# Kernel optimization log

Measured on AMD Instinct MI355X. Metric: run time of the kernel, lower is better.

The kernel has to match this reference:

```python
import jax, jax.numpy as jnp
import numpy as np

DIM = 768
H = 12          # num_heads
HD = DIM // H   # head_dim = 64
WS = 128        # window_size
SHIFT = 64      # shift_size
NPATCH = 128    # num_patches for relative bias
MLP = 3072
EPS = 1e-5


def _layernorm(x, w, b):
    m = jnp.mean(x, axis=-1, keepdims=True)
    v = jnp.mean(jnp.square(x - m), axis=-1, keepdims=True)
    return (x - m) * jax.lax.rsqrt(v + EPS) * w + b


def _window_attention(xw, mw, qkv_w, qkv_b, proj_w, proj_b, rel_bias):
    # xw: [Bw, ws, C] windows, mw: [Bw, ws] bool valid-key mask
    Bw, N, C = xw.shape
    qkv = (xw @ qkv_w + qkv_b).reshape(Bw, N, 3, H, HD)
    qkv = jnp.transpose(qkv, (2, 0, 3, 1, 4))  # [3, Bw, H, N, hd]
    q, k, v = qkv[0], qkv[1], qkv[2]
    attn = jnp.einsum('bhqd,bhkd->bhqk', q, k) * (HD ** -0.5)
    # relative position bias: table [2*NPATCH-1, H] gathered by index [N, N]
    coords = jnp.arange(N)
    rel_idx = coords[None, :] - coords[:, None] + (NPATCH - 1)  # [N, N]
    bias = jnp.transpose(rel_bias[rel_idx], (2, 0, 1))  # [H, N, N]
    attn = attn + bias[None]
    neg = jnp.finfo(attn.dtype).min
    attn = jnp.where(mw[:, None, None, :], attn, neg)  # mask invalid keys
    attn = jax.nn.softmax(attn, axis=-1)
    attn = jnp.nan_to_num(attn, nan=0.0)
    out = jnp.einsum('bhqk,bhkd->bqhd', attn, v).reshape(Bw, N, C)
    return out @ proj_w + proj_b


def reference(x, norm1_w, norm1_b, qkv_w, qkv_b, proj_w, proj_b, rel_bias,
              ls1, norm2_w, norm2_b, fc1_w, fc1_b, fc2_w, fc2_b, ls2):
    B, N, C = x.shape
    # ---- attention branch: norm1 -> shifted-window attention ----
    h = _layernorm(x, norm1_w, norm1_b)
    pad = (-N) % WS
    hp = jnp.pad(h, ((0, 0), (0, pad), (0, 0)))  # zero-pad sequence
    Npad = N + pad
    valid = jnp.broadcast_to(jnp.arange(Npad) < N, (B, Npad))
    if SHIFT > 0:
        hp = jnp.roll(hp, -SHIFT, axis=1)
        valid = jnp.roll(valid, -SHIFT, axis=1)
    nw = Npad // WS
    xw = hp.reshape(B * nw, WS, C)
    mw = valid.reshape(B * nw, WS)
    aw = _window_attention(xw, mw, qkv_w, qkv_b, proj_w, proj_b, rel_bias)
    a = aw.reshape(B, Npad, C)
    if SHIFT > 0:
        a = jnp.roll(a, SHIFT, axis=1)
    a = a[:, :N, :]
    x = x + a * ls1  # LayerScale, DropPath is identity
    # ---- MLP branch ----
    h2 = _layernorm(x, norm2_w, norm2_b)
    m = jax.nn.gelu(h2 @ fc1_w + fc1_b, approximate=False) @ fc2_w + fc2_b
    return x + m * ls2


def setup_inputs() -> dict:
    key = jax.random.key(0)
    ks = jax.random.split(key, 8)
    B, N = 16, 2000
    s = 0.02
    return {
        'x': jax.random.normal(ks[0], (B, N, DIM), jnp.float32),
        'norm1_w': jnp.ones((DIM,), jnp.float32),
        'norm1_b': jnp.zeros((DIM,), jnp.float32),
        'qkv_w': s * jax.random.normal(ks[1], (DIM, 3 * DIM), jnp.float32),
        'qkv_b': jnp.zeros((3 * DIM,), jnp.float32),
        'proj_w': s * jax.random.normal(ks[2], (DIM, DIM), jnp.float32),
        'proj_b': jnp.zeros((DIM,), jnp.float32),
        'rel_bias': s * jax.random.normal(ks[3], (2 * NPATCH - 1, H), jnp.float32),
        'ls1': 1e-5 * jnp.ones((DIM,), jnp.float32),
        'norm2_w': jnp.ones((DIM,), jnp.float32),
        'norm2_b': jnp.zeros((DIM,), jnp.float32),
        'fc1_w': s * jax.random.normal(ks[4], (DIM, MLP), jnp.float32),
        'fc1_b': jnp.zeros((MLP,), jnp.float32),
        'fc2_w': s * jax.random.normal(ks[5], (MLP, DIM), jnp.float32),
        'fc2_b': jnp.zeros((DIM,), jnp.float32),
        'ls2': 1e-5 * jnp.ones((DIM,), jnp.float32),
    }
```

## Files before the change

### kernel.cpp

```cpp
#include <hip/hip_runtime.h>
#include <hip/hip_bf16.h>

typedef unsigned short u16;
typedef unsigned char u8;
typedef __attribute__((ext_vector_type(8))) short bh8;
typedef __attribute__((ext_vector_type(4))) float fx4;
typedef __attribute__((ext_vector_type(4))) int i32x4;
typedef __attribute__((ext_vector_type(8))) int i32x8;

__device__ __forceinline__ u16 f2bf(float f) {
  union { float f; unsigned u; } v; v.f = f;
  unsigned r = v.u + 0x7FFFu + ((v.u >> 16) & 1u);
  return (u16)(r >> 16);
}

__device__ __forceinline__ u8 f2fp8(float x) {
  union { float f; unsigned u; } v; v.f = x;
  const unsigned sign = (v.u >> 24) & 0x80u;
  v.u &= 0x7FFFFFFFu;
  if (v.f >= 464.0f) return (u8)(sign | 0x7Eu);
  if (v.f < 0.015625f) {
    int q = (int)rintf(v.f * 512.0f);
    return (u8)(sign | (unsigned)q);
  }
  unsigned u2 = v.u + 0x7FFFFu + ((v.u >> 20) & 1u);
  unsigned e2 = (u2 >> 23) - 127u + 7u;
  unsigned mant = (u2 >> 20) & 7u;
  return (u8)(sign | (e2 << 3) | mant);
}

__device__ __forceinline__ void cvt2_fp8(float a, float b, u8& x, u8& y) {
#if __has_builtin(__builtin_amdgcn_cvt_pk_fp8_f32)
  int r = __builtin_amdgcn_cvt_pk_fp8_f32(a, b, 0, false);
  x = (u8)(r & 0xff);
  y = (u8)((r >> 8) & 0xff);
#else
  x = f2fp8(a);
  y = f2fp8(b);
#endif
}

__device__ __forceinline__ void gload_lds16(const void* g, void* l) {
  __builtin_amdgcn_global_load_lds(
      (const __attribute__((address_space(1))) void*)g,
      (__attribute__((address_space(3))) void*)l, 16, 0, 0);
}

__device__ __forceinline__ i32x8 rd32(const char* p0, const char* p1) {
  i32x4 lo = *(const i32x4*)p0;
  i32x4 hi = *(const i32x4*)p1;
  return __builtin_shufflevector(lo, hi, 0, 1, 2, 3, 4, 5, 6, 7);
}

__global__ __launch_bounds__(256) void transp_cvt(
    const float* __restrict__ W, u8* __restrict__ Wt, int K, int N) {
  __shared__ float tile[32][33];
  const int k0 = blockIdx.x * 32, n0 = blockIdx.y * 32;
  const int tx = threadIdx.x & 31, ty = threadIdx.x >> 5;
#pragma unroll
  for (int i = 0; i < 4; ++i)
    tile[ty + i * 8][tx] = W[(size_t)(k0 + ty + i * 8) * N + n0 + tx];
  __syncthreads();
#pragma unroll
  for (int i = 0; i < 4; ++i)
    Wt[(size_t)(n0 + ty + i * 8) * K + k0 + tx] = f2fp8(tile[tx][ty + i * 8] * 32.0f);
}

__device__ __forceinline__ float blockSum(float v, float* sh) {
#pragma unroll
  for (int m = 32; m; m >>= 1) v += __shfl_xor(v, m);
  if ((threadIdx.x & 63) == 0) sh[threadIdx.x >> 6] = v;
  __syncthreads();
  return sh[0] + sh[1] + sh[2] + sh[3];
}

__global__ __launch_bounds__(256) void ln1_k(
    const float* __restrict__ x, const float* __restrict__ w,
    const float* __restrict__ b, u8* __restrict__ hw) {
  __shared__ float sh1[4], sh2[4];
  const int row = blockIdx.x;
  const int bI = row >> 11, i = row & 2047;
  const int j = (i + 64) & 2047;
  const int tid = threadIdx.x;
  u8* dst = hw + (size_t)row * 768;
  if (j >= 2000) {
    dst[tid] = 0; dst[tid + 256] = 0; dst[tid + 512] = 0;
    return;
  }
  const float* xr = x + ((size_t)bI * 2000 + j) * 768;
  float v0 = xr[tid], v1 = xr[tid + 256], v2 = xr[tid + 512];
  float mean = blockSum(v0 + v1 + v2, sh1) * (1.0f / 768.0f);
  float d0 = v0 - mean, d1 = v1 - mean, d2 = v2 - mean;
  float var = blockSum(d0 * d0 + d1 * d1 + d2 * d2, sh2) * (1.0f / 768.0f);
  float rs = rsqrtf(var + 1e-5f);
  u8 x0, x1, x2, xd;
  cvt2_fp8((d0 * rs * w[tid] + b[tid]) * 4.0f,
           (d1 * rs * w[tid + 256] + b[tid + 256]) * 4.0f, x0, x1);
  cvt2_fp8((d2 * rs * w[tid + 512] + b[tid + 512]) * 4.0f, 0.0f, x2, xd);
  dst[tid] = x0; dst[tid + 256] = x1; dst[tid + 512] = x2;
}

__global__ __launch_bounds__(256) void ln2_k(
    const float* __restrict__ src, const float* __restrict__ w,
    const float* __restrict__ b, u8* __restrict__ dsth) {
  __shared__ float sh1[4], sh2[4];
  const int row = blockIdx.x;
  const int tid = threadIdx.x;
  const float* xr = src + (size_t)row * 768;
  u8* dst = dsth + (size_t)row * 768;
  float v0 = xr[tid], v1 = xr[tid + 256], v2 = xr[tid + 512];
  float mean = blockSum(v0 + v1 + v2, sh1) * (1.0f / 768.0f);
  float d0 = v0 - mean, d1 = v1 - mean, d2 = v2 - mean;
  float var = blockSum(d0 * d0 + d1 * d1 + d2 * d2, sh2) * (1.0f / 768.0f);
  float rs = rsqrtf(var + 1e-5f);
  u8 x0, x1, x2, xd;
  cvt2_fp8((d0 * rs * w[tid] + b[tid]) * 4.0f,
           (d1 * rs * w[tid + 256] + b[tid + 256]) * 4.0f, x0, x1);
  cvt2_fp8((d2 * rs * w[tid + 512] + b[tid + 512]) * 4.0f, 0.0f, x2, xd);
  dst[tid] = x0; dst[tid + 256] = x1; dst[tid + 512] = x2;
}

enum { EQKV = 0, EPROJ = 1, EFC1 = 2, EFC2 = 3 };

template <int EPI>
__global__ __launch_bounds__(256, 3) void gemm128f8(
    const u8* __restrict__ A, const u8* __restrict__ Bt,
    const float* __restrict__ bias, const float* __restrict__ lsv,
    const float* __restrict__ resid, float* __restrict__ outf,
    u16* __restrict__ outh, u8* __restrict__ outb,
    int gn, int N, int K, int mValid) {
  __shared__ u8 LDSBUF[32768];
  u8* As = LDSBUF;
  u8* Bs = LDSBUF + 16384;
  const int tid = threadIdx.x;
  const int lane = tid & 63, wid = tid >> 6;
  const int wr = wid >> 1, wc = wid & 1;

  const int nwg = gridDim.x, bid = blockIdx.x;
  const int q = nwg >> 3, r = nwg & 7;
  const int xcd = bid & 7, idx = bid >> 3;
  const int wg = (xcd < r ? xcd * (q + 1) : r * (q + 1) + (xcd - r) * q) + idx;
  const int mt = wg / gn, nt = wg % gn;
  const int m0 = mt * 128, n0 = nt * 128;
  const int NT = K >> 7;

  fx4 acc[4][4];
#pragma unroll
  for (int i = 0; i < 4; ++i)
#pragma unroll
    for (int j = 0; j < 4; ++j) acc[i][j] = fx4{0.f, 0.f, 0.f, 0.f};

  const int rsel = lane & 15, kgrp = lane >> 4;
  const int colb = kgrp * 32;
  const int xorc = (rsel & 7) << 4;

  const int rl = tid >> 3;
  const int kc16 = ((tid & 7) ^ (rl & 7)) * 16;
  const u8* aRow = A + (size_t)(m0 + rl) * K + kc16;
  const u8* bRow = Bt + (size_t)(n0 + rl) * K + kc16;

  for (int t = 0; t < NT; ++t) {
    const int k0 = t << 7;
#pragma unroll
    for (int i = 0; i < 4; ++i) {
      gload_lds16(aRow + (size_t)k0 + (size_t)(i * 32) * K,
                  (char*)As + i * 4096 + wid * 1024);
      gload_lds16(bRow + (size_t)k0 + (size_t)(i * 32) * K,
                  (char*)Bs + i * 4096 + wid * 1024);
    }
    __syncthreads();
    i32x8 af[4];
#pragma unroll
    for (int mi = 0; mi < 4; ++mi) {
      const char* ab = (const char*)As + (wr * 64 + mi * 16 + rsel) * 128;
      af[mi] = rd32(ab + (colb ^ xorc), ab + ((colb + 16) ^ xorc));
    }
#pragma unroll
    for (int ni = 0; ni < 4; ++ni) {
      const char* bb = (const char*)Bs + (wc * 64 + ni * 16 + rsel) * 128;
      i32x8 bfr = rd32(bb + (colb ^ xorc), bb + ((colb + 16) ^ xorc));
#pragma unroll
      for (int mi = 0; mi < 4; ++mi)
        acc[mi][ni] = __builtin_amdgcn_mfma_scale_f32_16x16x128_f8f6f4(
            af[mi], bfr, acc[mi][ni], 0, 0, 0, 125, 0, 122);
    }
    __syncthreads();
  }

  const int cc = lane & 15;
  const int rq = (lane >> 4) * 4;

  if (EPI == EQKV) {
    u16* Ls = (u16*)LDSBUF;
#pragma unroll
    for (int ni = 0; ni < 4; ++ni) {
      const int col = wc * 64 + ni * 16 + cc;
      const float bv = bias[n0 + col];
#pragma unroll
      for (int mi = 0; mi < 4; ++mi)
#pragma unroll
        for (int j = 0; j < 4; ++j)
          Ls[(wr * 64 + mi * 16 + rq + j) * 128 + col] = f2bf(acc[mi][ni][j] + bv);
    }
    __syncthreads();
#pragma unroll
    for (int i = 0; i < 8; ++i) {
      const int row = i * 16 + (tid >> 4);
      i32x4 v = *(const i32x4*)(LDSBUF + row * 256 + (tid & 15) * 16);
      *(i32x4*)(outh + (size_t)(m0 + row) * N + n0 + (tid & 15) * 8) = v;
    }
  } else if (EPI == EFC1) {
    u8* Ls = LDSBUF;
#pragma unroll
    for (int ni = 0; ni < 4; ++ni) {
      const int col = wc * 64 + ni * 16 + cc;
      const float bv = bias[n0 + col];
#pragma unroll
      for (int mi = 0; mi < 4; ++mi) {
#pragma unroll
        for (int jp = 0; jp < 2; ++jp) {
          const float va = acc[mi][ni][jp * 2] + bv;
          const float vb = acc[mi][ni][jp * 2 + 1] + bv;
          const float ga = va / (1.0f + __expf(-1.702f * va)) * 4.0f;
          const float gb = vb / (1.0f + __expf(-1.702f * vb)) * 4.0f;
          u8 xa, xb;
          cvt2_fp8(ga, gb, xa, xb);
          const int row = wr * 64 + mi * 16 + rq + jp * 2;
          Ls[row * 128 + col] = xa;
          Ls[(row + 1) * 128 + col] = xb;
        }
      }
    }
    __syncthreads();
#pragma unroll
    for (int i = 0; i < 4; ++i) {
      const int row = i * 32 + (tid >> 3);
      i32x4 v = *(const i32x4*)(Ls + row * 128 + (tid & 7) * 16);
      *(i32x4*)(outb + (size_t)(m0 + row) * N + n0 + (tid & 7) * 16) = v;
    }
  } else {
    float* Lf = (float*)LDSBUF;
#pragma unroll
    for (int p = 0; p < 2; ++p) {
      if (p) __syncthreads();
      if (wc == p) {
#pragma unroll
        for (int ni = 0; ni < 4; ++ni) {
          const int gc = n0 + p * 64 + ni * 16 + cc;
          const float bv = bias[gc], ls = lsv[gc];
#pragma unroll
          for (int mi = 0; mi < 4; ++mi)
#pragma unroll
            for (int j = 0; j < 4; ++j)
              Lf[(wr * 64 + mi * 16 + rq + j) * 64 + ni * 16 + cc] =
                  (acc[mi][ni][j] + bv) * ls;
        }
      }
      __syncthreads();
#pragma unroll
      for (int i = 0; i < 8; ++i) {
        const int row = i * 16 + (tid >> 4);
        const int gr = m0 + row;
        fx4 s = *(const fx4*)(Lf + row * 64 + (tid & 15) * 4);
        if (EPI == EFC2) {
          if (gr < mValid) {
            float* po = outf + (size_t)gr * 768 + n0 + p * 64 + (tid & 15) * 4;
            fx4 cur = *(const fx4*)po;
            *(fx4*)po = fx4{cur[0] + s[0], cur[1] + s[1], cur[2] + s[2], cur[3] + s[3]};
          }
        } else {
          const int bI = gr >> 11, ip = gr & 2047;
          const int jj = (ip + 64) & 2047;
          if (jj < 2000) {
            const size_t o = ((size_t)bI * 2000 + jj) * 768 + n0 + p * 64 + (tid & 15) * 4;
            fx4 rv = *(const fx4*)(resid + o);
            *(fx4*)(outf + o) = fx4{rv[0] + s[0], rv[1] + s[1], rv[2] + s[2], rv[3] + s[3]};
          }
        }
      }
    }
  }
}

struct AttnLds {
  union {
    struct { u16 Qs[128][72]; u16 Ks[128][72]; } qk;
    u16 Ps[128][136];
  } u;
  u16 Vt[64][136];
  float biasv[256];
};

__global__ __launch_bounds__(256, 2) void attn_k(
    const u16* __restrict__ qkv, const float* __restrict__ rel_bias,
    u8* __restrict__ aout) {
  __shared__ AttnLds L;
  const int blk = blockIdx.x;
  const int w = blk / 12, h = blk - w * 12;
  const int wi = w & 15;
  const int tid = threadIdx.x;
  const int lane = tid & 63, wid = tid >> 6;

  if (tid < 255) L.biasv[tid] = rel_bias[tid * 12 + h];

  const size_t rowbase = (size_t)w * 128;
#pragma unroll
  for (int i = 0; i < 4; ++i) {
    const int idx = tid + i * 256;
    const int r = idx >> 3, seg = idx & 7;
    const u16* src = qkv + (rowbase + r) * 2304 + h * 64 + seg * 8;
    *(bh8*)&L.u.qk.Qs[r][seg * 8] = *(const bh8*)(src);
    *(bh8*)&L.u.qk.Ks[r][seg * 8] = *(const bh8*)(src + 768);
    bh8 vv = *(const bh8*)(src + 1536);
#pragma unroll
    for (int e = 0; e < 8; ++e) L.Vt[seg * 8 + e][r] = ((const u16*)&vv)[e];
  }
  __syncthreads();

  const int R0 = wid * 32;
  const int rsel = lane & 15, kgrp = lane >> 4;
  fx4 s[2][8];
#pragma unroll
  for (int mi = 0; mi < 2; ++mi)
#pragma unroll
    for (int ni = 0; ni < 8; ++ni) s[mi][ni] = fx4{0.f, 0.f, 0.f, 0.f};

#pragma unroll
  for (int ks = 0; ks < 2; ++ks) {
    bh8 aq[2], bk[8];
#pragma unroll
    for (int mi = 0; mi < 2; ++mi)
      aq[mi] = *(const bh8*)&L.u.qk.Qs[R0 + mi * 16 + rsel][ks * 32 + kgrp * 8];
#pragma unroll
    for (int ni = 0; ni < 8; ++ni)
      bk[ni] = *(const bh8*)&L.u.qk.Ks[ni * 16 + rsel][ks * 32 + kgrp * 8];
#pragma unroll
    for (int mi = 0; mi < 2; ++mi)
#pragma unroll
      for (int ni = 0; ni < 8; ++ni)
        s[mi][ni] = __builtin_amdgcn_mfma_f32_16x16x32_bf16(aq[mi], bk[ni], s[mi][ni], 0, 0, 0);
  }

#pragma unroll
  for (int mi = 0; mi < 2; ++mi) {
#pragma unroll
    for (int j = 0; j < 4; ++j) {
      const int r = R0 + mi * 16 + kgrp * 4 + j;
      float vals[8];
      float mx = -1e30f;
#pragma unroll
      for (int ni = 0; ni < 8; ++ni) {
        const int c = ni * 16 + rsel;
        const int ic = wi * 128 + c;
        const bool valid = ((ic + 64) & 2047) < 2000;
        const float v = valid ? (s[mi][ni][j] * 0.125f + L.biasv[c - r + 127]) : -1e30f;
        vals[ni] = v;
        mx = fmaxf(mx, v);
      }
#pragma unroll
      for (int mm = 8; mm; mm >>= 1) mx = fmaxf(mx, __shfl_xor(mx, mm));
      float sum = 0.f;
#pragma unroll
      for (int ni = 0; ni < 8; ++ni) { float p = __expf(vals[ni] - mx); vals[ni] = p; sum += p; }
#pragma unroll
      for (int mm = 8; mm; mm >>= 1) sum += __shfl_xor(sum, mm);
      const float inv = 1.0f / sum;
#pragma unroll
      for (int ni = 0; ni < 8; ++ni) s[mi][ni][j] = vals[ni] * inv;
    }
  }
  __syncthreads();

#pragma unroll
  for (int mi = 0; mi < 2; ++mi)
#pragma unroll
    for (int ni = 0; ni < 8; ++ni)
#pragma unroll
      for (int j = 0; j < 4; ++j)
        L.u.Ps[R0 + mi * 16 + kgrp * 4 + j][ni * 16 + rsel] = f2bf(s[mi][ni][j]);
  __syncthreads();

  fx4 o[2][4];
#pragma unroll
  for (int mi = 0; mi < 2; ++mi)
#pragma unroll
    for (int ni = 0; ni < 4; ++ni) o[mi][ni] = fx4{0.f, 0.f, 0.f, 0.f};
#pragma unroll
  for (int ks = 0; ks < 4; ++ks) {
    bh8 ap[2], bv[4];
#pragma unroll
    for (int mi = 0; mi < 2; ++mi)
      ap[mi] = *(const bh8*)&L.u.Ps[R0 + mi * 16 + rsel][ks * 32 + kgrp * 8];
#pragma unroll
    for (int ni = 0; ni < 4; ++ni)
      bv[ni] = *(const bh8*)&L.Vt[ni * 16 + rsel][ks * 32 + kgrp * 8];
#pragma unroll
    for (int mi = 0; mi < 2; ++mi)
#pragma unroll
      for (int ni = 0; ni < 4; ++ni)
        o[mi][ni] = __builtin_amdgcn_mfma_f32_16x16x32_bf16(ap[mi], bv[ni], o[mi][ni], 0, 0, 0);
  }

#pragma unroll
  for (int mi = 0; mi < 2; ++mi)
#pragma unroll
    for (int ni = 0; ni < 4; ++ni)
#pragma unroll
      for (int jp = 0; jp < 2; ++jp) {
        u8 xa, xb;
        cvt2_fp8(o[mi][ni][jp * 2] * 4.0f, o[mi][ni][jp * 2 + 1] * 4.0f, xa, xb);
        const size_t r0 = rowbase + R0 + mi * 16 + kgrp * 4 + jp * 2;
        aout[r0 * 768 + h * 64 + ni * 16 + rsel] = xa;
        aout[(r0 + 1) * 768 + h * 64 + ni * 16 + rsel] = xb;
      }
}

extern "C" void kernel_launch(void* const* d_in, const int* in_sizes, int n_in,
                              void* d_out, int out_size, void* d_ws, size_t ws_size,
                              hipStream_t stream) {
  (void)in_sizes; (void)n_in; (void)out_size; (void)ws_size;
  const float* x        = (const float*)d_in[0];
  const float* n1w      = (const float*)d_in[1];
  const float* n1b      = (const float*)d_in[2];
  const float* qkv_w    = (const float*)d_in[3];
  const float* qkv_b    = (const float*)d_in[4];
  const float* proj_w   = (const float*)d_in[5];
  const float* proj_b   = (const float*)d_in[6];
  const float* rel_bias = (const float*)d_in[7];
  const float* ls1      = (const float*)d_in[8];
  const float* n2w      = (const float*)d_in[9];
  const float* n2b      = (const float*)d_in[10];
  const float* fc1_w    = (const float*)d_in[11];
  const float* fc1_b    = (const float*)d_in[12];
  const float* fc2_w    = (const float*)d_in[13];
  const float* fc2_b    = (const float*)d_in[14];
  const float* ls2      = (const float*)d_in[15];
  float* out = (float*)d_out;

  char* ws = (char*)d_ws;
  u8*  WtQ   = (u8*)(ws);
  u8*  WtP   = (u8*)(ws + 3538944);
  u8*  WtF1  = (u8*)(ws + 4718592);
  u8*  WtF2  = (u8*)(ws + 9437184);
  u8*  bufB8 = (u8*)(ws + 14155776);
  char* bufA = ws + 14155776 + 50331648;
  u16* bufA16 = (u16*)bufA;
  u8*  bufA8  = (u8*)bufA;

  dim3 t256(256);
  transp_cvt<<<dim3(24, 72), t256, 0, stream>>>(qkv_w, WtQ, 768, 2304);
  transp_cvt<<<dim3(24, 24), t256, 0, stream>>>(proj_w, WtP, 768, 768);
  transp_cvt<<<dim3(24, 96), t256, 0, stream>>>(fc1_w, WtF1, 768, 3072);
  transp_cvt<<<dim3(96, 24), t256, 0, stream>>>(fc2_w, WtF2, 3072, 768);

  ln1_k<<<32768, t256, 0, stream>>>(x, n1w, n1b, bufB8);
  gemm128f8<EQKV><<<dim3(256 * 18), t256, 0, stream>>>(
      bufB8, WtQ, qkv_b, nullptr, nullptr, nullptr, bufA16, nullptr, 18, 2304, 768, 32768);
  attn_k<<<3072, t256, 0, stream>>>(bufA16, rel_bias, bufB8);
  gemm128f8<EPROJ><<<dim3(256 * 6), t256, 0, stream>>>(
      bufB8, WtP, proj_b, ls1, x, out, nullptr, nullptr, 6, 768, 768, 32768);
  ln2_k<<<32000, t256, 0, stream>>>(out, n2w, n2b, bufB8);
  gemm128f8<EFC1><<<dim3(250 * 24), t256, 0, stream>>>(
      bufB8, WtF1, fc1_b, nullptr, nullptr, nullptr, nullptr, bufA8, 24, 3072, 768, 32000);
  gemm128f8<EFC2><<<dim3(250 * 6), t256, 0, stream>>>(
      bufA8, WtF2, fc2_b, ls2, nullptr, out, nullptr, nullptr, 6, 768, 3072, 32000);
}
```

Baseline: 505.9 us.

## Store QKV as FP8 and use 256-row tiles for the FC1 GEMM

The QKV GEMM epilogue now writes FP8 (scaled by 4) instead of BF16, halving the QKV intermediate traffic. The attention kernel decodes the FP8 values back to BF16 when it loads them into shared memory. A new FC1 kernel uses 512 threads and 256x128 tiles so each B tile is reused across twice as many rows, which cuts B loads and block count. In exchange, Q/K/V carry extra FP8 quantization error and attention does more conversion work at load time.

```diff
diff --git a/kernel.cpp b/kernel.cpp
--- a/kernel.cpp
+++ b/kernel.cpp
@@ -37,6 +37,33 @@
 #else
   x = f2fp8(a);
   y = f2fp8(b);
+#endif
+}
+
+__device__ __forceinline__ float fp8_manual(u8 b) {
+  unsigned s = b >> 7, e = (b >> 3) & 15, m = b & 7;
+  float v;
+  if (e == 0) {
+    v = m * 0.001953125f;
+  } else {
+    union { unsigned u; float f; } t;
+    t.u = ((e + 120u) << 23) | (m << 20);
+    v = t.f;
+  }
+  return s ? -v : v;
+}
+
+__device__ __forceinline__ void fp8dec4(unsigned w, float* o) {
+#if __has_builtin(__builtin_amdgcn_cvt_f32_fp8)
+  o[0] = __builtin_amdgcn_cvt_f32_fp8((int)w, 0);
+  o[1] = __builtin_amdgcn_cvt_f32_fp8((int)w, 1);
+  o[2] = __builtin_amdgcn_cvt_f32_fp8((int)w, 2);
+  o[3] = __builtin_amdgcn_cvt_f32_fp8((int)w, 3);
+#else
+  o[0] = fp8_manual((u8)(w & 0xffu));
+  o[1] = fp8_manual((u8)((w >> 8) & 0xffu));
+  o[2] = fp8_manual((u8)((w >> 16) & 0xffu));
+  o[3] = fp8_manual((u8)((w >> 24) & 0xffu));
 #endif
 }
 
@@ -120,14 +147,14 @@
   dst[tid] = x0; dst[tid + 256] = x1; dst[tid + 512] = x2;
 }
 
-enum { EQKV = 0, EPROJ = 1, EFC1 = 2, EFC2 = 3 };
+enum { EQKV = 0, EPROJ = 1, EFC2 = 3 };
 
 template <int EPI>
 __global__ __launch_bounds__(256, 3) void gemm128f8(
     const u8* __restrict__ A, const u8* __restrict__ Bt,
     const float* __restrict__ bias, const float* __restrict__ lsv,
     const float* __restrict__ resid, float* __restrict__ outf,
-    u16* __restrict__ outh, u8* __restrict__ outb,
+    u8* __restrict__ outb,
     int gn, int N, int K, int mValid) {
   __shared__ u8 LDSBUF[32768];
   u8* As = LDSBUF;
@@ -191,40 +218,18 @@
   const int rq = (lane >> 4) * 4;
 
   if (EPI == EQKV) {
-    u16* Ls = (u16*)LDSBUF;
+    u8* Ls = LDSBUF;
 #pragma unroll
     for (int ni = 0; ni < 4; ++ni) {
       const int col = wc * 64 + ni * 16 + cc;
       const float bv = bias[n0 + col];
 #pragma unroll
-      for (int mi = 0; mi < 4; ++mi)
-#pragma unroll
-        for (int j = 0; j < 4; ++j)
-          Ls[(wr * 64 + mi * 16 + rq + j) * 128 + col] = f2bf(acc[mi][ni][j] + bv);
-    }
-    __syncthreads();
-#pragma unroll
-    for (int i = 0; i < 8; ++i) {
-      const int row = i * 16 + (tid >> 4);
-      i32x4 v = *(const i32x4*)(LDSBUF + row * 256 + (tid & 15) * 16);
-      *(i32x4*)(outh + (size_t)(m0 + row) * N + n0 + (tid & 15) * 8) = v;
-    }
-  } else if (EPI == EFC1) {
-    u8* Ls = LDSBUF;
-#pragma unroll
-    for (int ni = 0; ni < 4; ++ni) {
-      const int col = wc * 64 + ni * 16 + cc;
-      const float bv = bias[n0 + col];
-#pragma unroll
       for (int mi = 0; mi < 4; ++mi) {
 #pragma unroll
         for (int jp = 0; jp < 2; ++jp) {
-          const float va = acc[mi][ni][jp * 2] + bv;
-          const float vb = acc[mi][ni][jp * 2 + 1] + bv;
-          const float ga = va / (1.0f + __expf(-1.702f * va)) * 4.0f;
-          const float gb = vb / (1.0f + __expf(-1.702f * vb)) * 4.0f;
           u8 xa, xb;
-          cvt2_fp8(ga, gb, xa, xb);
+          cvt2_fp8((acc[mi][ni][jp * 2] + bv) * 4.0f,
+                   (acc[mi][ni][jp * 2 + 1] + bv) * 4.0f, xa, xb);
           const int row = wr * 64 + mi * 16 + rq + jp * 2;
           Ls[row * 128 + col] = xa;
           Ls[(row + 1) * 128 + col] = xb;
@@ -282,6 +287,108 @@
   }
 }
 
+__global__ __launch_bounds__(512, 4) void gemm256fc1(
+    const u8* __restrict__ A, const u8* __restrict__ Bt,
+    const float* __restrict__ bias, u8* __restrict__ outb,
+    int gn, int N, int K) {
+  __shared__ u8 LDSBUF[49152];
+  u8* As0 = LDSBUF;
+  u8* As1 = LDSBUF + 16384;
+  u8* Bs  = LDSBUF + 32768;
+  const int tid = threadIdx.x;
+  const int lane = tid & 63, wid = tid >> 6;
+  const int wr = wid >> 1, wc = wid & 1;
+
+  const int nwg = gridDim.x, bid = blockIdx.x;
+  const int q = nwg >> 3, r = nwg & 7;
+  const int xcd = bid & 7, idx = bid >> 3;
+  const int wg = (xcd < r ? xcd * (q + 1) : r * (q + 1) + (xcd - r) * q) + idx;
+  const int mt = wg / gn, nt = wg % gn;
+  const int m0 = mt * 256, n0 = nt * 128;
+  const int NT = K >> 7;
+
+  fx4 acc[4][4];
+#pragma unroll
+  for (int i = 0; i < 4; ++i)
+#pragma unroll
+    for (int j = 0; j < 4; ++j) acc[i][j] = fx4{0.f, 0.f, 0.f, 0.f};
+
+  const int rsel = lane & 15, kgrp = lane >> 4;
+  const int colb = kgrp * 32;
+  const int xorc = (rsel & 7) << 4;
+
+  const int c0 = wid * 128 + lane;
+  const int c1 = c0 + 64;
+  const int r0_ = c0 >> 3, k0c = ((c0 & 7) ^ (r0_ & 7)) * 16;
+  const int r1_ = c1 >> 3, k1c = ((c1 & 7) ^ (r1_ & 7)) * 16;
+  const int d0 = wid * 2048, d1 = wid * 2048 + 1024;
+
+  const u8* Alo = A + (size_t)m0 * K;
+  const u8* Ahi = A + (size_t)(m0 + 128) * K;
+  const u8* Bp  = Bt + (size_t)n0 * K;
+
+  u8* Amine = (wr < 2) ? As0 : As1;
+  const int wrl = wr & 1;
+
+  for (int t = 0; t < NT; ++t) {
+    const int k0 = t << 7;
+    gload_lds16(Alo + (size_t)r0_ * K + k0 + k0c, (char*)As0 + d0);
+    gload_lds16(Alo + (size_t)r1_ * K + k0 + k1c, (char*)As0 + d1);
+    gload_lds16(Ahi + (size_t)r0_ * K + k0 + k0c, (char*)As1 + d0);
+    gload_lds16(Ahi + (size_t)r1_ * K + k0 + k1c, (char*)As1 + d1);
+    gload_lds16(Bp  + (size_t)r0_ * K + k0 + k0c, (char*)Bs + d0);
+    gload_lds16(Bp  + (size_t)r1_ * K + k0 + k1c, (char*)Bs + d1);
+    __syncthreads();
+    i32x8 af[4];
+#pragma unroll
+    for (int mi = 0; mi < 4; ++mi) {
+      const char* ab = (const char*)Amine + (wrl * 64 + mi * 16 + rsel) * 128;
+      af[mi] = rd32(ab + (colb ^ xorc), ab + ((colb + 16) ^ xorc));
+    }
+#pragma unroll
+    for (int ni = 0; ni < 4; ++ni) {
+      const char* bb = (const char*)Bs + (wc * 64 + ni * 16 + rsel) * 128;
+      i32x8 bfr = rd32(bb + (colb ^ xorc), bb + ((colb + 16) ^ xorc));
+#pragma unroll
+      for (int mi = 0; mi < 4; ++mi)
+        acc[mi][ni] = __builtin_amdgcn_mfma_scale_f32_16x16x128_f8f6f4(
+            af[mi], bfr, acc[mi][ni], 0, 0, 0, 125, 0, 122);
+    }
+    __syncthreads();
+  }
+
+  const int cc = lane & 15;
+  const int rq = (lane >> 4) * 4;
+  u8* Ls = LDSBUF;
+#pragma unroll
+  for (int ni = 0; ni < 4; ++ni) {
+    const int col = wc * 64 + ni * 16 + cc;
+    const float bv = bias[n0 + col];
+#pragma unroll
+    for (int mi = 0; mi < 4; ++mi) {
+#pragma unroll
+      for (int jp = 0; jp < 2; ++jp) {
+        const float va = acc[mi][ni][jp * 2] + bv;
+        const float vb = acc[mi][ni][jp * 2 + 1] + bv;
+        const float ga = va / (1.0f + __expf(-1.702f * va)) * 4.0f;
+        const float gb = vb / (1.0f + __expf(-1.702f * vb)) * 4.0f;
+        u8 xa, xb;
+        cvt2_fp8(ga, gb, xa, xb);
+        const int row = wr * 64 + mi * 16 + rq + jp * 2;
+        Ls[row * 128 + col] = xa;
+        Ls[(row + 1) * 128 + col] = xb;
+      }
+    }
+  }
+  __syncthreads();
+#pragma unroll
+  for (int i = 0; i < 4; ++i) {
+    const int row = i * 64 + (tid >> 3);
+    i32x4 v = *(const i32x4*)(Ls + row * 128 + (tid & 7) * 16);
+    *(i32x4*)(outb + (size_t)(m0 + row) * N + n0 + (tid & 7) * 16) = v;
+  }
+}
+
 struct AttnLds {
   union {
     struct { u16 Qs[128][72]; u16 Ks[128][72]; } qk;
@@ -292,7 +399,7 @@
 };
 
 __global__ __launch_bounds__(256, 2) void attn_k(
-    const u16* __restrict__ qkv, const float* __restrict__ rel_bias,
+    const u8* __restrict__ qkv8, const float* __restrict__ rel_bias,
     u8* __restrict__ aout) {
   __shared__ AttnLds L;
   const int blk = blockIdx.x;
@@ -308,12 +415,29 @@
   for (int i = 0; i < 4; ++i) {
     const int idx = tid + i * 256;
     const int r = idx >> 3, seg = idx & 7;
-    const u16* src = qkv + (rowbase + r) * 2304 + h * 64 + seg * 8;
-    *(bh8*)&L.u.qk.Qs[r][seg * 8] = *(const bh8*)(src);
-    *(bh8*)&L.u.qk.Ks[r][seg * 8] = *(const bh8*)(src + 768);
-    bh8 vv = *(const bh8*)(src + 1536);
-#pragma unroll
-    for (int e = 0; e < 8; ++e) L.Vt[seg * 8 + e][r] = ((const u16*)&vv)[e];
+    const u8* src = qkv8 + (rowbase + r) * 2304 + h * 64 + seg * 8;
+    unsigned qlo = *(const unsigned*)(src);
+    unsigned qhi = *(const unsigned*)(src + 4);
+    unsigned klo = *(const unsigned*)(src + 768);
+    unsigned khi = *(const unsigned*)(src + 772);
+    unsigned vlo = *(const unsigned*)(src + 1536);
+    unsigned vhi = *(const unsigned*)(src + 1540);
+    float qf[8], kf[8], vf[8];
+    fp8dec4(qlo, qf); fp8dec4(qhi, qf + 4);
+    fp8dec4(klo, kf); fp8dec4(khi, kf + 4);
+    fp8dec4(vlo, vf); fp8dec4(vhi, vf + 4);
+    bh8 qv, kv;
+    u16 va[8];
+#pragma unroll
+    for (int e = 0; e < 8; ++e) {
+      qv[e] = (short)f2bf(qf[e] * 0.25f);
+      kv[e] = (short)f2bf(kf[e] * 0.25f);
+      va[e] = f2bf(vf[e] * 0.25f);
+    }
+    *(bh8*)&L.u.qk.Qs[r][seg * 8] = qv;
+    *(bh8*)&L.u.qk.Ks[r][seg * 8] = kv;
+#pragma unroll
+    for (int e = 0; e < 8; ++e) L.Vt[seg * 8 + e][r] = va[e];
   }
   __syncthreads();
 
@@ -443,9 +567,7 @@
   u8*  WtF1  = (u8*)(ws + 4718592);
   u8*  WtF2  = (u8*)(ws + 9437184);
   u8*  bufB8 = (u8*)(ws + 14155776);
-  char* bufA = ws + 14155776 + 50331648;
-  u16* bufA16 = (u16*)bufA;
-  u8*  bufA8  = (u8*)bufA;
+  u8*  bufA8 = (u8*)(ws + 14155776 + 50331648);
 
   dim3 t256(256);
   transp_cvt<<<dim3(24, 72), t256, 0, stream>>>(qkv_w, WtQ, 768, 2304);
@@ -455,13 +577,13 @@
 
   ln1_k<<<32768, t256, 0, stream>>>(x, n1w, n1b, bufB8);
   gemm128f8<EQKV><<<dim3(256 * 18), t256, 0, stream>>>(
-      bufB8, WtQ, qkv_b, nullptr, nullptr, nullptr, bufA16, nullptr, 18, 2304, 768, 32768);
-  attn_k<<<3072, t256, 0, stream>>>(bufA16, rel_bias, bufB8);
+      bufB8, WtQ, qkv_b, nullptr, nullptr, nullptr, bufA8, 18, 2304, 768, 32768);
+  attn_k<<<3072, t256, 0, stream>>>(bufA8, rel_bias, bufB8);
   gemm128f8<EPROJ><<<dim3(256 * 6), t256, 0, stream>>>(
-      bufB8, WtP, proj_b, ls1, x, out, nullptr, nullptr, 6, 768, 768, 32768);
+      bufB8, WtP, proj_b, ls1, x, out, nullptr, 6, 768, 768, 32768);
   ln2_k<<<32000, t256, 0, stream>>>(out, n2w, n2b, bufB8);
-  gemm128f8<EFC1><<<dim3(250 * 24), t256, 0, stream>>>(
-      bufB8, WtF1, fc1_b, nullptr, nullptr, nullptr, nullptr, bufA8, 24, 3072, 768, 32000);
+  gemm256fc1<<<dim3(125 * 24), dim3(512), 0, stream>>>(
+      bufB8, WtF1, fc1_b, bufA8, 24, 3072, 768);
   gemm128f8<EFC2><<<dim3(250 * 6), t256, 0, stream>>>(
-      bufA8, WtF2, fc2_b, ls2, nullptr, out, nullptr, nullptr, 6, 768, 3072, 32000);
-}
+      bufA8, WtF2, fc2_b, ls2, nullptr, out, nullptr, 6, 768, 3072, 32000);
+}
```

After: 518.5 us. +2.5%, slower.

## Store QKV activations as FP8 and raise GEMM occupancy bound

Applied to the files above, without the earlier changes.

The QKV GEMM epilogue now writes FP8, scaled by 4, instead of bf16, sharing the FC1 epilogue path. The attention kernel loads FP8 Q/K/V, decodes them to float, rescales and converts to bf16 in LDS. This halves the QKV intermediate traffic between the two kernels but loses precision in Q/K/V. The GEMM launch bound also rises from 3 to 5 blocks per SM, which may add register pressure or spills.

```diff
diff --git a/kernel.cpp b/kernel.cpp
--- a/kernel.cpp
+++ b/kernel.cpp
@@ -37,6 +37,33 @@
 #else
   x = f2fp8(a);
   y = f2fp8(b);
+#endif
+}
+
+__device__ __forceinline__ float fp8_manual(u8 b) {
+  unsigned s = b >> 7, e = (b >> 3) & 15, m = b & 7;
+  float v;
+  if (e == 0) {
+    v = m * 0.001953125f;
+  } else {
+    union { unsigned u; float f; } t;
+    t.u = ((e + 120u) << 23) | (m << 20);
+    v = t.f;
+  }
+  return s ? -v : v;
+}
+
+__device__ __forceinline__ void fp8dec4(unsigned w, float* o) {
+#if __has_builtin(__builtin_amdgcn_cvt_f32_fp8)
+  o[0] = __builtin_amdgcn_cvt_f32_fp8((int)w, 0);
+  o[1] = __builtin_amdgcn_cvt_f32_fp8((int)w, 1);
+  o[2] = __builtin_amdgcn_cvt_f32_fp8((int)w, 2);
+  o[3] = __builtin_amdgcn_cvt_f32_fp8((int)w, 3);
+#else
+  o[0] = fp8_manual((u8)(w & 0xffu));
+  o[1] = fp8_manual((u8)((w >> 8) & 0xffu));
+  o[2] = fp8_manual((u8)((w >> 16) & 0xffu));
+  o[3] = fp8_manual((u8)((w >> 24) & 0xffu));
 #endif
 }
 
@@ -123,11 +150,11 @@
 enum { EQKV = 0, EPROJ = 1, EFC1 = 2, EFC2 = 3 };
 
 template <int EPI>
-__global__ __launch_bounds__(256, 3) void gemm128f8(
+__global__ __launch_bounds__(256, 5) void gemm128f8(
     const u8* __restrict__ A, const u8* __restrict__ Bt,
     const float* __restrict__ bias, const float* __restrict__ lsv,
     const float* __restrict__ resid, float* __restrict__ outf,
-    u16* __restrict__ outh, u8* __restrict__ outb,
+    u8* __restrict__ outb,
     int gn, int N, int K, int mValid) {
   __shared__ u8 LDSBUF[32768];
   u8* As = LDSBUF;
@@ -190,41 +217,24 @@
   const int cc = lane & 15;
   const int rq = (lane >> 4) * 4;
 
-  if (EPI == EQKV) {
-    u16* Ls = (u16*)LDSBUF;
+  if (EPI == EQKV || EPI == EFC1) {
+    u8* Ls = LDSBUF;
 #pragma unroll
     for (int ni = 0; ni < 4; ++ni) {
       const int col = wc * 64 + ni * 16 + cc;
       const float bv = bias[n0 + col];
 #pragma unroll
-      for (int mi = 0; mi < 4; ++mi)
-#pragma unroll
-        for (int j = 0; j < 4; ++j)
-          Ls[(wr * 64 + mi * 16 + rq + j) * 128 + col] = f2bf(acc[mi][ni][j] + bv);
-    }
-    __syncthreads();
-#pragma unroll
-    for (int i = 0; i < 8; ++i) {
-      const int row = i * 16 + (tid >> 4);
-      i32x4 v = *(const i32x4*)(LDSBUF + row * 256 + (tid & 15) * 16);
-      *(i32x4*)(outh + (size_t)(m0 + row) * N + n0 + (tid & 15) * 8) = v;
-    }
-  } else if (EPI == EFC1) {
-    u8* Ls = LDSBUF;
-#pragma unroll
-    for (int ni = 0; ni < 4; ++ni) {
-      const int col = wc * 64 + ni * 16 + cc;
-      const float bv = bias[n0 + col];
-#pragma unroll
       for (int mi = 0; mi < 4; ++mi) {
 #pragma unroll
         for (int jp = 0; jp < 2; ++jp) {
-          const float va = acc[mi][ni][jp * 2] + bv;
-          const float vb = acc[mi][ni][jp * 2 + 1] + bv;
-          const float ga = va / (1.0f + __expf(-1.702f * va)) * 4.0f;
-          const float gb = vb / (1.0f + __expf(-1.702f * vb)) * 4.0f;
+          float va = acc[mi][ni][jp * 2] + bv;
+          float vb = acc[mi][ni][jp * 2 + 1] + bv;
+          if (EPI == EFC1) {
+            va = va / (1.0f + __expf(-1.702f * va));
+            vb = vb / (1.0f + __expf(-1.702f * vb));
+          }
           u8 xa, xb;
-          cvt2_fp8(ga, gb, xa, xb);
+          cvt2_fp8(va * 4.0f, vb * 4.0f, xa, xb);
           const int row = wr * 64 + mi * 16 + rq + jp * 2;
           Ls[row * 128 + col] = xa;
           Ls[(row + 1) * 128 + col] = xb;
@@ -292,7 +302,7 @@
 };
 
 __global__ __launch_bounds__(256, 2) void attn_k(
-    const u16* __restrict__ qkv, const float* __restrict__ rel_bias,
+    const u8* __restrict__ qkv8, const float* __restrict__ rel_bias,
     u8* __restrict__ aout) {
   __shared__ AttnLds L;
   const int blk = blockIdx.x;
@@ -308,12 +318,29 @@
   for (int i = 0; i < 4; ++i) {
     const int idx = tid + i * 256;
     const int r = idx >> 3, seg = idx & 7;
-    const u16* src = qkv + (rowbase + r) * 2304 + h * 64 + seg * 8;
-    *(bh8*)&L.u.qk.Qs[r][seg * 8] = *(const bh8*)(src);
-    *(bh8*)&L.u.qk.Ks[r][seg * 8] = *(const bh8*)(src + 768);
-    bh8 vv = *(const bh8*)(src + 1536);
-#pragma unroll
-    for (int e = 0; e < 8; ++e) L.Vt[seg * 8 + e][r] = ((const u16*)&vv)[e];
+    const u8* src = qkv8 + (rowbase + r) * 2304 + h * 64 + seg * 8;
+    unsigned qlo = *(const unsigned*)(src);
+    unsigned qhi = *(const unsigned*)(src + 4);
+    unsigned klo = *(const unsigned*)(src + 768);
+    unsigned khi = *(const unsigned*)(src + 772);
+    unsigned vlo = *(const unsigned*)(src + 1536);
+    unsigned vhi = *(const unsigned*)(src + 1540);
+    float qf[8], kf[8], vf[8];
+    fp8dec4(qlo, qf); fp8dec4(qhi, qf + 4);
+    fp8dec4(klo, kf); fp8dec4(khi, kf + 4);
+    fp8dec4(vlo, vf); fp8dec4(vhi, vf + 4);
+    bh8 qv, kv;
+    u16 va[8];
+#pragma unroll
+    for (int e = 0; e < 8; ++e) {
+      qv[e] = (short)f2bf(qf[e] * 0.25f);
+      kv[e] = (short)f2bf(kf[e] * 0.25f);
+      va[e] = f2bf(vf[e] * 0.25f);
+    }
+    *(bh8*)&L.u.qk.Qs[r][seg * 8] = qv;
+    *(bh8*)&L.u.qk.Ks[r][seg * 8] = kv;
+#pragma unroll
+    for (int e = 0; e < 8; ++e) L.Vt[seg * 8 + e][r] = va[e];
   }
   __syncthreads();
 
@@ -443,9 +470,7 @@
   u8*  WtF1  = (u8*)(ws + 4718592);
   u8*  WtF2  = (u8*)(ws + 9437184);
   u8*  bufB8 = (u8*)(ws + 14155776);
-  char* bufA = ws + 14155776 + 50331648;
-  u16* bufA16 = (u16*)bufA;
-  u8*  bufA8  = (u8*)bufA;
+  u8*  bufA8 = (u8*)(ws + 14155776 + 50331648);
 
   dim3 t256(256);
   transp_cvt<<<dim3(24, 72), t256, 0, stream>>>(qkv_w, WtQ, 768, 2304);
@@ -455,13 +480,13 @@
 
   ln1_k<<<32768, t256, 0, stream>>>(x, n1w, n1b, bufB8);
   gemm128f8<EQKV><<<dim3(256 * 18), t256, 0, stream>>>(
-      bufB8, WtQ, qkv_b, nullptr, nullptr, nullptr, bufA16, nullptr, 18, 2304, 768, 32768);
-  attn_k<<<3072, t256, 0, stream>>>(bufA16, rel_bias, bufB8);
+      bufB8, WtQ, qkv_b, nullptr, nullptr, nullptr, bufA8, 18, 2304, 768, 32768);
+  attn_k<<<3072, t256, 0, stream>>>(bufA8, rel_bias, bufB8);
   gemm128f8<EPROJ><<<dim3(256 * 6), t256, 0, stream>>>(
-      bufB8, WtP, proj_b, ls1, x, out, nullptr, nullptr, 6, 768, 768, 32768);
+      bufB8, WtP, proj_b, ls1, x, out, nullptr, 6, 768, 768, 32768);
   ln2_k<<<32000, t256, 0, stream>>>(out, n2w, n2b, bufB8);
   gemm128f8<EFC1><<<dim3(250 * 24), t256, 0, stream>>>(
-      bufB8, WtF1, fc1_b, nullptr, nullptr, nullptr, nullptr, bufA8, 24, 3072, 768, 32000);
+      bufB8, WtF1, fc1_b, nullptr, nullptr, nullptr, bufA8, 24, 3072, 768, 32000);
   gemm128f8<EFC2><<<dim3(250 * 6), t256, 0, stream>>>(
-      bufA8, WtF2, fc2_b, ls2, nullptr, out, nullptr, nullptr, 6, 768, 3072, 32000);
-}
+      bufA8, WtF2, fc2_b, ls2, nullptr, out, nullptr, 6, 768, 3072, 32000);
+}
```

After: 1.815 ms. 259% more time.
